# Kernel optimization log

Measured on AMD Instinct MI355X. Metric: run time of the kernel, lower is better.

Reference implementation:

```python
import jax, jax.numpy as jnp
import numpy as np

HIDDEN = 1024
BATCH = 32
STEPS = 2048


def setup_inputs() -> dict:
    key = jax.random.key(0)
    k1, k2, k3, k4, k5 = jax.random.split(key, 5)
    query = jax.random.normal(k1, (BATCH, HIDDEN), dtype=jnp.float32)
    keys = jax.random.normal(k2, (BATCH, STEPS, HIDDEN), dtype=jnp.float32)
    # nn.Linear weights, stored as (out, in); init scale ~ 1/sqrt(in)
    s = 1.0 / np.sqrt(HIDDEN)
    W_query = jax.random.uniform(k3, (HIDDEN, HIDDEN), jnp.float32, -s, s)
    W_key = jax.random.uniform(k4, (HIDDEN, HIDDEN), jnp.float32, -s, s)
    V = jax.random.uniform(k5, (1, HIDDEN), jnp.float32, -s, s)
    return {"query": query, "keys": keys, "W_query": W_query, "W_key": W_key, "V": V}


def reference(query, keys, W_query, W_key, V):
    # q_proj: (B, H); k_proj: (B, S, H)
    q_proj = query @ W_query.T
    k_proj = jnp.einsum('bsh,oh->bso', keys, W_key)
    # additive score: V^T tanh(Wq q + Wk k) -> (B, S)
    scores = jnp.einsum('bsh,h->bs', jnp.tanh(q_proj[:, None, :] + k_proj), V[0])
    weights = jax.nn.softmax(scores, axis=-1)
    context = jnp.einsum('bs,bsh->bh', weights, keys)
    return context, weights
```

## Files before the change

kernel.cpp:

```cpp
#include <hip/hip_runtime.h>
#include <hip/hip_bf16.h>
#include <stdint.h>

#define HID 1024
#define NB 32
#define NS 2048
#define NROWS (NB*NS)

typedef short v8s __attribute__((ext_vector_type(8)));
typedef float v16f __attribute__((ext_vector_type(16)));

__device__ __forceinline__ unsigned cvt2(float a, float b){
  unsigned r;
  asm("v_cvt_pk_bf16_f32 %0, %1, %2" : "=v"(r) : "v"(a), "v"(b));
  return r;
}

__device__ __forceinline__ uint4 pack8(const float4& a, const float4& b){
  uint4 r;
  r.x = cvt2(a.x, a.y);
  r.y = cvt2(a.z, a.w);
  r.z = cvt2(b.x, b.y);
  r.w = cvt2(b.z, b.w);
  return r;
}

__global__ __launch_bounds__(256) void k_qproj(const float* __restrict__ query,
                                               const float* __restrict__ Wq,
                                               float* __restrict__ qp,
                                               float* __restrict__ scores){
  int tid = threadIdx.x;
  int gw = ((blockIdx.x << 8) + tid) >> 6;
  int lane = tid & 63;
  int b = gw >> 10, o = gw & 1023;
  const float* qr = query + b*HID;
  const float* wr = Wq + (size_t)o*HID;
  float p = 0.f;
#pragma unroll
  for (int i = 0; i < 16; ++i){
    int h = lane + (i << 6);
    p += qr[h]*wr[h];
  }
#pragma unroll
  for (int m = 32; m >= 1; m >>= 1) p += __shfl_xor(p, m, 64);
  if (lane == 0) qp[gw] = p;
  if (tid < 8) scores[(blockIdx.x << 3) + tid] = 0.f;
}

__global__ __launch_bounds__(256) void k_scores(const float* __restrict__ keys,
                                                const float* __restrict__ Wk,
                                                const float* __restrict__ qp,
                                                const float* __restrict__ V,
                                                float* __restrict__ scores){
  __shared__ uint4 Ab[2][1024];
  __shared__ uint4 Bb[2][1024];
  int bid = blockIdx.x;
  int v = ((bid & 7) << 9) | (bid >> 3);
  int mt = v >> 3, nt = v & 7;
  int m0 = mt << 7, n0 = nt << 7;
  int b = m0 >> 11;
  int tid = threadIdx.x;
  int lane = tid & 63;
  int wid = tid >> 6;
  int wm = wid >> 1, wn = wid & 1;
  int l31 = lane & 31, hi = lane >> 5;

  int skg[4], srw[4];
#pragma unroll
  for (int i = 0; i < 4; ++i){
    int sidx = (i << 8) + tid;
    skg[i] = sidx & 7;
    srw[i] = sidx >> 3;
  }
  float4 ar[4][2], br[4][2];

  auto loadt = [&](int kt){
#pragma unroll
    for (int i = 0; i < 4; ++i){
      const float* as = keys + (size_t)(m0 + srw[i])*HID + (kt << 6) + (skg[i] << 3);
      ar[i][0] = *(const float4*)as;
      ar[i][1] = *(const float4*)(as + 4);
      const float* bs2 = Wk + (size_t)(n0 + srw[i])*HID + (kt << 6) + (skg[i] << 3);
      br[i][0] = *(const float4*)bs2;
      br[i][1] = *(const float4*)(bs2 + 4);
    }
  };
  auto writet = [&](int bsel){
#pragma unroll
    for (int i = 0; i < 4; ++i){
      int slot = (skg[i] << 7) | (srw[i] ^ skg[i]);
      Ab[bsel][slot] = pack8(ar[i][0], ar[i][1]);
      Bb[bsel][slot] = pack8(br[i][0], br[i][1]);
    }
  };

  v16f acc[2][2] = {};

  loadt(0);
  writet(0);
  __syncthreads();
  for (int kt = 0; kt < 16; ++kt){
    int bs = kt & 1;
    if (kt < 15) loadt(kt + 1);
#pragma unroll
    for (int ks = 0; ks < 4; ++ks){
      int kg = (ks << 1) + hi;
      int rsw = l31 ^ kg;
      int abase = (kg << 7) + (wm << 6) + rsw;
      int bbase = (kg << 7) + (wn << 6) + rsw;
      v8s a0 = __builtin_bit_cast(v8s, Ab[bs][abase]);
      v8s a1 = __builtin_bit_cast(v8s, Ab[bs][abase + 32]);
      v8s b0 = __builtin_bit_cast(v8s, Bb[bs][bbase]);
      v8s b1 = __builtin_bit_cast(v8s, Bb[bs][bbase + 32]);
      acc[0][0] = __builtin_amdgcn_mfma_f32_32x32x16_bf16(a0, b0, acc[0][0], 0, 0, 0);
      acc[0][1] = __builtin_amdgcn_mfma_f32_32x32x16_bf16(a0, b1, acc[0][1], 0, 0, 0);
      acc[1][0] = __builtin_amdgcn_mfma_f32_32x32x16_bf16(a1, b0, acc[1][0], 0, 0, 0);
      acc[1][1] = __builtin_amdgcn_mfma_f32_32x32x16_bf16(a1, b1, acc[1][1], 0, 0, 0);
    }
    if (kt < 15){
      __syncthreads();
      writet(bs ^ 1);
      __syncthreads();
    }
  }

  float qpv[2], Vv[2];
#pragma unroll
  for (int ni = 0; ni < 2; ++ni){
    int o = n0 + (wn << 6) + (ni << 5) + l31;
    qpv[ni] = qp[(b << 10) + o];
    Vv[ni] = V[o];
  }
#pragma unroll
  for (int mi = 0; mi < 2; ++mi){
#pragma unroll
    for (int r = 0; r < 16; ++r){
      float sp = 0.f;
#pragma unroll
      for (int ni = 0; ni < 2; ++ni){
        float x = qpv[ni] + acc[mi][ni][r];
        float e = __expf(2.f*x);
        sp += Vv[ni]*(1.f - 2.f/(e + 1.f));
      }
#pragma unroll
      for (int m = 16; m >= 1; m >>= 1) sp += __shfl_xor(sp, m, 64);
      if (l31 == 0){
        int row = m0 + (wm << 6) + (mi << 5) + (r & 3) + ((r >> 2) << 3) + (hi << 2);
        atomicAdd(&scores[row], sp);
      }
    }
  }
}

__global__ __launch_bounds__(256) void k_softmax(const float* __restrict__ scores,
                                                 float* __restrict__ out){
  int b = blockIdx.x; int tid = threadIdx.x;
  __shared__ float red[8];
  const float* srow = scores + b*NS;
  float vv[8];
  float mx = -1e30f;
#pragma unroll
  for (int i = 0; i < 8; ++i){ vv[i] = srow[tid + (i << 8)]; mx = fmaxf(mx, vv[i]); }
#pragma unroll
  for (int m = 32; m >= 1; m >>= 1) mx = fmaxf(mx, __shfl_xor(mx, m, 64));
  int wid = tid >> 6, lane = tid & 63;
  if (lane == 0) red[wid] = mx;
  __syncthreads();
  mx = fmaxf(fmaxf(red[0], red[1]), fmaxf(red[2], red[3]));
  float s = 0.f;
#pragma unroll
  for (int i = 0; i < 8; ++i){ vv[i] = __expf(vv[i] - mx); s += vv[i]; }
#pragma unroll
  for (int m = 32; m >= 1; m >>= 1) s += __shfl_xor(s, m, 64);
  if (lane == 0) red[4 + wid] = s;
  __syncthreads();
  s = red[4] + red[5] + red[6] + red[7];
  float inv = 1.f/s;
  float* wout = out + NB*HID + b*NS;
#pragma unroll
  for (int i = 0; i < 8; ++i) wout[tid + (i << 8)] = vv[i]*inv;
  float4* ctx = (float4*)(out + b*HID);
  ctx[tid] = make_float4(0.f, 0.f, 0.f, 0.f);
}

__global__ __launch_bounds__(256) void k_context(const float* __restrict__ keys,
                                                 const float* __restrict__ w,
                                                 float* __restrict__ ctx){
  int blk = blockIdx.x;
  int b = blk >> 5;
  int hc = (blk >> 3) & 3;
  int sc = blk & 7;
  int h = (hc << 8) + threadIdx.x;
  const float* wrow = w + b*NS + (sc << 8);
  const float* krow = keys + ((size_t)b*NS + (sc << 8))*HID + h;
  float a = 0.f;
#pragma unroll 4
  for (int s = 0; s < 256; ++s) a += wrow[s]*krow[(size_t)s*HID];
  atomicAdd(&ctx[b*HID + h], a);
}

extern "C" void kernel_launch(void* const* d_in, const int* in_sizes, int n_in,
                              void* d_out, int out_size, void* d_ws, size_t ws_size,
                              hipStream_t stream){
  const float* query = (const float*)d_in[0];
  const float* keys  = (const float*)d_in[1];
  const float* Wq    = (const float*)d_in[2];
  const float* Wk    = (const float*)d_in[3];
  const float* V     = (const float*)d_in[4];
  float* out = (float*)d_out;
  float* qp = (float*)d_ws;
  float* scores = qp + NB*HID;

  hipLaunchKernelGGL(k_qproj,   dim3(8192), dim3(256), 0, stream, query, Wq, qp, scores);
  hipLaunchKernelGGL(k_scores,  dim3(4096), dim3(256), 0, stream, keys, Wk, qp, V, scores);
  hipLaunchKernelGGL(k_softmax, dim3(32),   dim3(256), 0, stream, scores, out);
  hipLaunchKernelGGL(k_context, dim3(1024), dim3(256), 0, stream, keys, out + NB*HID, out);
}
```

Baseline: 774.4 us.

## Pre-convert keys and Wk to bf16, load tiles via global_load_lds, vectorize context

Adds a conversion pass that writes keys and W_key to bf16 in the workspace. The score GEMM then streams bf16 tiles straight into LDS with global_load_lds, dropping the per-tile fp32 register staging and in-kernel packing, and uses single-buffered LDS with 4 blocks per CU. The context kernel is rewritten to read keys as float4 with the weights cached in shared memory. The conversion adds an extra full read of fp32 keys plus a bf16 write, and the new GEMM loop no longer overlaps loads with MFMA inside a block. A fallback keeps the old path when the workspace is too small.

```diff
diff --git a/kernel.cpp b/kernel.cpp
--- a/kernel.cpp
+++ b/kernel.cpp
@@ -5,10 +5,15 @@
 #define HID 1024
 #define NB 32
 #define NS 2048
-#define NROWS (NB*NS)
 
 typedef short v8s __attribute__((ext_vector_type(8)));
 typedef float v16f __attribute__((ext_vector_type(16)));
+typedef const __attribute__((address_space(1))) void* gas_t;
+typedef __attribute__((address_space(3))) void* las_t;
+
+__device__ __forceinline__ void gload16(const void* g, void* l){
+  __builtin_amdgcn_global_load_lds((gas_t)g, (las_t)l, 16, 0, 0);
+}
 
 __device__ __forceinline__ unsigned cvt2(float a, float b){
   unsigned r;
@@ -23,6 +28,17 @@
   r.z = cvt2(b.x, b.y);
   r.w = cvt2(b.z, b.w);
   return r;
+}
+
+__global__ __launch_bounds__(256) void k_conv(const float* __restrict__ src,
+                                              ushort* __restrict__ dst, int n8){
+  int i0 = (blockIdx.x << 8) + threadIdx.x;
+  int stride = gridDim.x << 8;
+  for (int i = i0; i < n8; i += stride){
+    const float4* s = (const float4*)(src + (size_t)i*8);
+    float4 a = s[0], b = s[1];
+    *(uint4*)(dst + (size_t)i*8) = pack8(a, b);
+  }
 }
 
 __global__ __launch_bounds__(256) void k_qproj(const float* __restrict__ query,
@@ -47,11 +63,91 @@
   if (tid < 8) scores[(blockIdx.x << 3) + tid] = 0.f;
 }
 
-__global__ __launch_bounds__(256) void k_scores(const float* __restrict__ keys,
-                                                const float* __restrict__ Wk,
-                                                const float* __restrict__ qp,
-                                                const float* __restrict__ V,
-                                                float* __restrict__ scores){
+__global__ __launch_bounds__(256, 4) void k_scores2(const ushort* __restrict__ keysb,
+                                                    const ushort* __restrict__ Wkb,
+                                                    const float* __restrict__ qp,
+                                                    const float* __restrict__ V,
+                                                    float* __restrict__ scores){
+  __shared__ uint4 Ab[1024];
+  __shared__ uint4 Bb[1024];
+  int bid = blockIdx.x;
+  int v = ((bid & 7) << 9) | (bid >> 3);
+  int mt = v >> 3, nt = v & 7;
+  int m0 = mt << 7, n0 = nt << 7;
+  int b = m0 >> 11;
+  int tid = threadIdx.x;
+  int lane = tid & 63;
+  int wid = tid >> 6;
+  int wm = wid >> 1, wn = wid & 1;
+  int l31 = lane & 31, hi = lane >> 5;
+
+  v16f acc[2][2] = {};
+
+  for (int kt = 0; kt < 16; ++kt){
+#pragma unroll
+    for (int j = 0; j < 4; ++j){
+      int s = (wid << 8) + (j << 6) + lane;
+      int row = s >> 3;
+      int lc = (s & 7) ^ (row & 7);
+      size_t goff = (size_t)row*HID + (kt << 6) + (lc << 3);
+      char* lb = (char*)Ab + (((wid << 2) + j) << 10);
+      gload16(keysb + (size_t)m0*HID + goff, lb);
+      char* lb2 = (char*)Bb + (((wid << 2) + j) << 10);
+      gload16(Wkb + (size_t)n0*HID + goff, lb2);
+    }
+    __syncthreads();
+#pragma unroll
+    for (int ks = 0; ks < 4; ++ks){
+      int kg = (ks << 1) + hi;
+      int ra = (wm << 6) + l31;
+      int rb = (wn << 6) + l31;
+      int offA = ra*128 + ((kg ^ (ra & 7)) << 4);
+      int offB = rb*128 + ((kg ^ (rb & 7)) << 4);
+      v8s a0 = __builtin_bit_cast(v8s, *(const uint4*)((const char*)Ab + offA));
+      v8s a1 = __builtin_bit_cast(v8s, *(const uint4*)((const char*)Ab + offA + 4096));
+      v8s b0 = __builtin_bit_cast(v8s, *(const uint4*)((const char*)Bb + offB));
+      v8s b1 = __builtin_bit_cast(v8s, *(const uint4*)((const char*)Bb + offB + 4096));
+      acc[0][0] = __builtin_amdgcn_mfma_f32_32x32x16_bf16(a0, b0, acc[0][0], 0, 0, 0);
+      acc[0][1] = __builtin_amdgcn_mfma_f32_32x32x16_bf16(a0, b1, acc[0][1], 0, 0, 0);
+      acc[1][0] = __builtin_amdgcn_mfma_f32_32x32x16_bf16(a1, b0, acc[1][0], 0, 0, 0);
+      acc[1][1] = __builtin_amdgcn_mfma_f32_32x32x16_bf16(a1, b1, acc[1][1], 0, 0, 0);
+    }
+    __syncthreads();
+  }
+
+  float qpv[2], Vv[2];
+#pragma unroll
+  for (int ni = 0; ni < 2; ++ni){
+    int o = n0 + (wn << 6) + (ni << 5) + l31;
+    qpv[ni] = qp[(b << 10) + o];
+    Vv[ni] = V[o];
+  }
+#pragma unroll
+  for (int mi = 0; mi < 2; ++mi){
+#pragma unroll
+    for (int r = 0; r < 16; ++r){
+      float sp = 0.f;
+#pragma unroll
+      for (int ni = 0; ni < 2; ++ni){
+        float x = qpv[ni] + acc[mi][ni][r];
+        float e = __expf(2.f*x);
+        sp += Vv[ni]*(1.f - 2.f/(e + 1.f));
+      }
+#pragma unroll
+      for (int m = 16; m >= 1; m >>= 1) sp += __shfl_xor(sp, m, 64);
+      if (l31 == 0){
+        int row = m0 + (wm << 6) + (mi << 5) + (r & 3) + ((r >> 2) << 3) + (hi << 2);
+        atomicAdd(&scores[row], sp);
+      }
+    }
+  }
+}
+
+__global__ __launch_bounds__(256) void k_scores_fb(const float* __restrict__ keys,
+                                                   const float* __restrict__ Wk,
+                                                   const float* __restrict__ qp,
+                                                   const float* __restrict__ V,
+                                                   float* __restrict__ scores){
   __shared__ uint4 Ab[2][1024];
   __shared__ uint4 Bb[2][1024];
   int bid = blockIdx.x;
@@ -73,7 +169,6 @@
     srw[i] = sidx >> 3;
   }
   float4 ar[4][2], br[4][2];
-
   auto loadt = [&](int kt){
 #pragma unroll
     for (int i = 0; i < 4; ++i){
@@ -93,12 +188,8 @@
       Bb[bsel][slot] = pack8(br[i][0], br[i][1]);
     }
   };
-
   v16f acc[2][2] = {};
-
-  loadt(0);
-  writet(0);
-  __syncthreads();
+  loadt(0); writet(0); __syncthreads();
   for (int kt = 0; kt < 16; ++kt){
     int bs = kt & 1;
     if (kt < 15) loadt(kt + 1);
@@ -123,7 +214,6 @@
       __syncthreads();
     }
   }
-
   float qpv[2], Vv[2];
 #pragma unroll
   for (int ni = 0; ni < 2; ++ni){
@@ -183,20 +273,26 @@
   ctx[tid] = make_float4(0.f, 0.f, 0.f, 0.f);
 }
 
-__global__ __launch_bounds__(256) void k_context(const float* __restrict__ keys,
-                                                 const float* __restrict__ w,
-                                                 float* __restrict__ ctx){
+__global__ __launch_bounds__(256) void k_context2(const float* __restrict__ keys,
+                                                  const float* __restrict__ w,
+                                                  float* __restrict__ ctx){
+  __shared__ float ws[128];
   int blk = blockIdx.x;
-  int b = blk >> 5;
-  int hc = (blk >> 3) & 3;
-  int sc = blk & 7;
-  int h = (hc << 8) + threadIdx.x;
-  const float* wrow = w + b*NS + (sc << 8);
-  const float* krow = keys + ((size_t)b*NS + (sc << 8))*HID + h;
-  float a = 0.f;
-#pragma unroll 4
-  for (int s = 0; s < 256; ++s) a += wrow[s]*krow[(size_t)s*HID];
-  atomicAdd(&ctx[b*HID + h], a);
+  int b = blk >> 4, sc = blk & 15;
+  int s0 = sc << 7;
+  int tid = threadIdx.x;
+  if (tid < 128) ws[tid] = w[b*NS + s0 + tid];
+  __syncthreads();
+  const float4* kp = (const float4*)(keys + ((size_t)b*NS + s0)*HID) + tid;
+  float4 a = make_float4(0.f, 0.f, 0.f, 0.f);
+#pragma unroll 8
+  for (int s = 0; s < 128; ++s){
+    float4 kv = kp[(size_t)s*256];
+    float wv = ws[s];
+    a.x += wv*kv.x; a.y += wv*kv.y; a.z += wv*kv.z; a.w += wv*kv.w;
+  }
+  float* o = ctx + b*HID + (tid << 2);
+  atomicAdd(o, a.x); atomicAdd(o + 1, a.y); atomicAdd(o + 2, a.z); atomicAdd(o + 3, a.w);
 }
 
 extern "C" void kernel_launch(void* const* d_in, const int* in_sizes, int n_in,
@@ -210,9 +306,19 @@
   float* out = (float*)d_out;
   float* qp = (float*)d_ws;
   float* scores = qp + NB*HID;
-
-  hipLaunchKernelGGL(k_qproj,   dim3(8192), dim3(256), 0, stream, query, Wq, qp, scores);
-  hipLaunchKernelGGL(k_scores,  dim3(4096), dim3(256), 0, stream, keys, Wk, qp, V, scores);
-  hipLaunchKernelGGL(k_softmax, dim3(32),   dim3(256), 0, stream, scores, out);
-  hipLaunchKernelGGL(k_context, dim3(1024), dim3(256), 0, stream, keys, out + NB*HID, out);
-}
+  ushort* keysb = (ushort*)((char*)d_ws + ((size_t)NB*HID + (size_t)NB*NS)*4);
+  ushort* Wkb = keysb + (size_t)NB*NS*HID;
+  const size_t WS_NEED = ((size_t)NB*HID + (size_t)NB*NS)*4
+                       + ((size_t)NB*NS*HID + (size_t)HID*HID)*2;
+
+  hipLaunchKernelGGL(k_qproj, dim3(8192), dim3(256), 0, stream, query, Wq, qp, scores);
+  if (ws_size >= WS_NEED){
+    hipLaunchKernelGGL(k_conv, dim3(2048), dim3(256), 0, stream, keys, keysb, NB*NS*HID/8);
+    hipLaunchKernelGGL(k_conv, dim3(256),  dim3(256), 0, stream, Wk, Wkb, HID*HID/8);
+    hipLaunchKernelGGL(k_scores2, dim3(4096), dim3(256), 0, stream, keysb, Wkb, qp, V, scores);
+  } else {
+    hipLaunchKernelGGL(k_scores_fb, dim3(4096), dim3(256), 0, stream, keys, Wk, qp, V, scores);
+  }
+  hipLaunchKernelGGL(k_softmax, dim3(32), dim3(256), 0, stream, scores, out);
+  hipLaunchKernelGGL(k_context2, dim3(512), dim3(256), 0, stream, keys, out + NB*HID, out);
+}
```

Result: faster. 681.1 us (-12.0%).

## Pre-convert keys and Wk to bf16, stage GEMM tiles via direct global-to-LDS loads

Applied to the files above, without the earlier changes.

Adds a conversion pass that writes keys and W_key as bf16 into the workspace. The score GEMM then streams bf16 tiles straight into LDS with global_load_lds in a depth-2 pipeline with explicit waitcnt and barriers, replacing register-staged fp32 loads and in-loop packing. The context kernel is reorganised so each block reads whole rows as float4 with weights held in shared memory. This costs an extra full read and half-size write of keys (256 MB in, 128 MB out) in exchange for halving the GEMM's repeated key reads across the 8 N-tiles.

```diff
diff --git a/kernel.cpp b/kernel.cpp
--- a/kernel.cpp
+++ b/kernel.cpp
@@ -5,10 +5,15 @@
 #define HID 1024
 #define NB 32
 #define NS 2048
-#define NROWS (NB*NS)
 
 typedef short v8s __attribute__((ext_vector_type(8)));
 typedef float v16f __attribute__((ext_vector_type(16)));
+typedef const __attribute__((address_space(1))) void* gas_t;
+typedef __attribute__((address_space(3))) void* las_t;
+
+__device__ __forceinline__ void gload16(const void* g, void* l){
+  __builtin_amdgcn_global_load_lds((gas_t)g, (las_t)l, 16, 0, 0);
+}
 
 __device__ __forceinline__ unsigned cvt2(float a, float b){
   unsigned r;
@@ -23,6 +28,17 @@
   r.z = cvt2(b.x, b.y);
   r.w = cvt2(b.z, b.w);
   return r;
+}
+
+__global__ __launch_bounds__(256) void k_conv(const float* __restrict__ src,
+                                              ushort* __restrict__ dst, int n8){
+  int i0 = (blockIdx.x << 8) + threadIdx.x;
+  int stride = gridDim.x << 8;
+  for (int i = i0; i < n8; i += stride){
+    const float4* s = (const float4*)(src + (size_t)i*8);
+    float4 a = s[0], b = s[1];
+    *(uint4*)(dst + (size_t)i*8) = pack8(a, b);
+  }
 }
 
 __global__ __launch_bounds__(256) void k_qproj(const float* __restrict__ query,
@@ -47,11 +63,11 @@
   if (tid < 8) scores[(blockIdx.x << 3) + tid] = 0.f;
 }
 
-__global__ __launch_bounds__(256) void k_scores(const float* __restrict__ keys,
-                                                const float* __restrict__ Wk,
-                                                const float* __restrict__ qp,
-                                                const float* __restrict__ V,
-                                                float* __restrict__ scores){
+__global__ __launch_bounds__(256, 2) void k_scores2(const ushort* __restrict__ keysb,
+                                                    const ushort* __restrict__ Wkb,
+                                                    const float* __restrict__ qp,
+                                                    const float* __restrict__ V,
+                                                    float* __restrict__ scores){
   __shared__ uint4 Ab[2][1024];
   __shared__ uint4 Bb[2][1024];
   int bid = blockIdx.x;
@@ -65,63 +81,54 @@
   int wm = wid >> 1, wn = wid & 1;
   int l31 = lane & 31, hi = lane >> 5;
 
-  int skg[4], srw[4];
-#pragma unroll
-  for (int i = 0; i < 4; ++i){
-    int sidx = (i << 8) + tid;
-    skg[i] = sidx & 7;
-    srw[i] = sidx >> 3;
-  }
-  float4 ar[4][2], br[4][2];
-
-  auto loadt = [&](int kt){
-#pragma unroll
-    for (int i = 0; i < 4; ++i){
-      const float* as = keys + (size_t)(m0 + srw[i])*HID + (kt << 6) + (skg[i] << 3);
-      ar[i][0] = *(const float4*)as;
-      ar[i][1] = *(const float4*)(as + 4);
-      const float* bs2 = Wk + (size_t)(n0 + srw[i])*HID + (kt << 6) + (skg[i] << 3);
-      br[i][0] = *(const float4*)bs2;
-      br[i][1] = *(const float4*)(bs2 + 4);
+  v16f acc[2][2] = {};
+
+  auto stage = [&](int kt, int bsel){
+#pragma unroll
+    for (int j = 0; j < 4; ++j){
+      int s = (wid << 8) + (j << 6) + lane;
+      int row = s >> 3;
+      int lc = (s & 7) ^ (row & 7);
+      size_t goff = (size_t)row*HID + (kt << 6) + (lc << 3);
+      char* lb = (char*)(&Ab[bsel][0]) + (((wid << 2) + j) << 10);
+      gload16(keysb + (size_t)m0*HID + goff, lb);
+      char* lb2 = (char*)(&Bb[bsel][0]) + (((wid << 2) + j) << 10);
+      gload16(Wkb + (size_t)n0*HID + goff, lb2);
     }
   };
-  auto writet = [&](int bsel){
-#pragma unroll
-    for (int i = 0; i < 4; ++i){
-      int slot = (skg[i] << 7) | (srw[i] ^ skg[i]);
-      Ab[bsel][slot] = pack8(ar[i][0], ar[i][1]);
-      Bb[bsel][slot] = pack8(br[i][0], br[i][1]);
-    }
-  };
-
-  v16f acc[2][2] = {};
-
-  loadt(0);
-  writet(0);
-  __syncthreads();
+
+  stage(0, 0);
+  stage(1, 1);
   for (int kt = 0; kt < 16; ++kt){
     int bs = kt & 1;
-    if (kt < 15) loadt(kt + 1);
+    if (kt < 15) asm volatile("s_waitcnt vmcnt(8)" ::: "memory");
+    else         asm volatile("s_waitcnt vmcnt(0)" ::: "memory");
+    __builtin_amdgcn_sched_barrier(0);
+    __builtin_amdgcn_s_barrier();
+    __builtin_amdgcn_sched_barrier(0);
 #pragma unroll
     for (int ks = 0; ks < 4; ++ks){
       int kg = (ks << 1) + hi;
-      int rsw = l31 ^ kg;
-      int abase = (kg << 7) + (wm << 6) + rsw;
-      int bbase = (kg << 7) + (wn << 6) + rsw;
-      v8s a0 = __builtin_bit_cast(v8s, Ab[bs][abase]);
-      v8s a1 = __builtin_bit_cast(v8s, Ab[bs][abase + 32]);
-      v8s b0 = __builtin_bit_cast(v8s, Bb[bs][bbase]);
-      v8s b1 = __builtin_bit_cast(v8s, Bb[bs][bbase + 32]);
+      int ra = (wm << 6) + l31;
+      int rb = (wn << 6) + l31;
+      int offA = ra*128 + ((kg ^ (ra & 7)) << 4);
+      int offB = rb*128 + ((kg ^ (rb & 7)) << 4);
+      const char* Abase = (const char*)(&Ab[bs][0]);
+      const char* Bbase = (const char*)(&Bb[bs][0]);
+      v8s a0 = __builtin_bit_cast(v8s, *(const uint4*)(Abase + offA));
+      v8s a1 = __builtin_bit_cast(v8s, *(const uint4*)(Abase + offA + 4096));
+      v8s b0 = __builtin_bit_cast(v8s, *(const uint4*)(Bbase + offB));
+      v8s b1 = __builtin_bit_cast(v8s, *(const uint4*)(Bbase + offB + 4096));
       acc[0][0] = __builtin_amdgcn_mfma_f32_32x32x16_bf16(a0, b0, acc[0][0], 0, 0, 0);
       acc[0][1] = __builtin_amdgcn_mfma_f32_32x32x16_bf16(a0, b1, acc[0][1], 0, 0, 0);
       acc[1][0] = __builtin_amdgcn_mfma_f32_32x32x16_bf16(a1, b0, acc[1][0], 0, 0, 0);
       acc[1][1] = __builtin_amdgcn_mfma_f32_32x32x16_bf16(a1, b1, acc[1][1], 0, 0, 0);
     }
-    if (kt < 15){
-      __syncthreads();
-      writet(bs ^ 1);
-      __syncthreads();
-    }
+    asm volatile("s_waitcnt lgkmcnt(0)" ::: "memory");
+    __builtin_amdgcn_sched_barrier(0);
+    __builtin_amdgcn_s_barrier();
+    __builtin_amdgcn_sched_barrier(0);
+    if (kt < 14) stage(kt + 2, bs);
   }
 
   float qpv[2], Vv[2];
@@ -183,20 +190,26 @@
   ctx[tid] = make_float4(0.f, 0.f, 0.f, 0.f);
 }
 
-__global__ __launch_bounds__(256) void k_context(const float* __restrict__ keys,
-                                                 const float* __restrict__ w,
-                                                 float* __restrict__ ctx){
+__global__ __launch_bounds__(256) void k_context2(const float* __restrict__ keys,
+                                                  const float* __restrict__ w,
+                                                  float* __restrict__ ctx){
+  __shared__ float ws[64];
   int blk = blockIdx.x;
-  int b = blk >> 5;
-  int hc = (blk >> 3) & 3;
-  int sc = blk & 7;
-  int h = (hc << 8) + threadIdx.x;
-  const float* wrow = w + b*NS + (sc << 8);
-  const float* krow = keys + ((size_t)b*NS + (sc << 8))*HID + h;
-  float a = 0.f;
-#pragma unroll 4
-  for (int s = 0; s < 256; ++s) a += wrow[s]*krow[(size_t)s*HID];
-  atomicAdd(&ctx[b*HID + h], a);
+  int b = blk >> 5, sc = blk & 31;
+  int s0 = sc << 6;
+  int tid = threadIdx.x;
+  if (tid < 64) ws[tid] = w[b*NS + s0 + tid];
+  __syncthreads();
+  const float4* kp = (const float4*)(keys + ((size_t)b*NS + s0)*HID) + tid;
+  float4 a = make_float4(0.f, 0.f, 0.f, 0.f);
+#pragma unroll 8
+  for (int s = 0; s < 64; ++s){
+    float4 kv = kp[(size_t)s*256];
+    float wv = ws[s];
+    a.x += wv*kv.x; a.y += wv*kv.y; a.z += wv*kv.z; a.w += wv*kv.w;
+  }
+  float* o = ctx + b*HID + (tid << 2);
+  atomicAdd(o, a.x); atomicAdd(o + 1, a.y); atomicAdd(o + 2, a.z); atomicAdd(o + 3, a.w);
 }
 
 extern "C" void kernel_launch(void* const* d_in, const int* in_sizes, int n_in,
@@ -210,9 +223,13 @@
   float* out = (float*)d_out;
   float* qp = (float*)d_ws;
   float* scores = qp + NB*HID;
-
-  hipLaunchKernelGGL(k_qproj,   dim3(8192), dim3(256), 0, stream, query, Wq, qp, scores);
-  hipLaunchKernelGGL(k_scores,  dim3(4096), dim3(256), 0, stream, keys, Wk, qp, V, scores);
-  hipLaunchKernelGGL(k_softmax, dim3(32),   dim3(256), 0, stream, scores, out);
-  hipLaunchKernelGGL(k_context, dim3(1024), dim3(256), 0, stream, keys, out + NB*HID, out);
-}
+  ushort* keysb = (ushort*)((char*)d_ws + ((size_t)NB*HID + (size_t)NB*NS)*4);
+  ushort* Wkb = keysb + (size_t)NB*NS*HID;
+
+  hipLaunchKernelGGL(k_qproj, dim3(8192), dim3(256), 0, stream, query, Wq, qp, scores);
+  hipLaunchKernelGGL(k_conv, dim3(2048), dim3(256), 0, stream, keys, keysb, NB*NS*HID/8);
+  hipLaunchKernelGGL(k_conv, dim3(256),  dim3(256), 0, stream, Wk, Wkb, HID*HID/8);
+  hipLaunchKernelGGL(k_scores2, dim3(4096), dim3(256), 0, stream, keysb, Wkb, qp, V, scores);
+  hipLaunchKernelGGL(k_softmax, dim3(32), dim3(256), 0, stream, scores, out);
+  hipLaunchKernelGGL(k_context2, dim3(1024), dim3(256), 0, stream, keys, out + NB*HID, out);
+}
```

After: 762.0 us. About the same (-1.6%).
